# Optimization experiments

Measured on AMD Instinct MI355X. Metric: run time of the kernel, lower is better.

## Reference

```python
import jax, jax.numpy as jnp
from jax import lax
import numpy as np

B, DIM, H, W = 1, 48, 192, 192
HEADS, K, DIL = 2, 7, 3
HD = DIM // HEADS
HID = int(DIM * 2.66)  # 127 (Restormer GEGLU hidden)
EPS = 1e-5


def _window_starts(L, Kk, D):
    # NATTEN window-start rule: keep phase i % D, shift window inside bounds.
    s = np.zeros(L, dtype=np.int32)
    for i in range(L):
        if D <= 1:
            st = max(i - Kk // 2, 0)
            if i + Kk // 2 >= L:
                st = L - Kk
        else:
            st = i - (Kk // 2) * D
            if st < 0:
                st = i % D
            elif i + (Kk // 2) * D >= L:
                imodd = i % D
                a = (L // D) * D
                b = L - a
                if imodd < b:
                    st = L - b + imodd - 2 * (Kk // 2) * D
                else:
                    st = a + imodd - Kk * D
        s[i] = st
    return s


def _nbr_tables(L, Kk, D):
    st = _window_starts(L, Kk, D)
    idx = st[:, None] + np.arange(Kk)[None, :] * D          # [L, K] absolute neighbor idx
    pb = (st - np.arange(L)) // D                            # signed offset of window start (in dilation units)
    pb = pb[:, None] + (Kk - 1) + np.arange(Kk)[None, :]     # [L, K] rpb index in [0, 2K-2]
    return jnp.asarray(idx), jnp.asarray(pb)

IH, PBH = _nbr_tables(H, K, DIL)
IW, PBW = _nbr_tables(W, K, DIL)


def layernorm(x, w, b):  # channel LN on NCHW (WithBias, biased var)
    mu = x.mean(1, keepdims=True)
    var = ((x - mu) ** 2).mean(1, keepdims=True)
    return (x - mu) / jnp.sqrt(var + EPS) * w[None, :, None, None] + b[None, :, None, None]


def na2d(x, qkv_w, qkv_b, rpb, proj_w, proj_b):
    # x: NCHW -> BHWC
    t = x.transpose(0, 2, 3, 1)
    qkv = t @ qkv_w.T + qkv_b                                # [B,H,W,3*DIM]
    qkv = qkv.reshape(B, H, W, 3, HEADS, HD)
    q, k, v = qkv[:, :, :, 0], qkv[:, :, :, 1], qkv[:, :, :, 2]
    q = q * (HD ** -0.5)
    # gather dilated 7x7 neighborhoods: [B, H, K, W, K, heads, hd]
    kn = k[:, IH[:, :, None, None], IW[None, None, :, :]]
    vn = v[:, IH[:, :, None, None], IW[None, None, :, :]]
    attn = jnp.einsum('bijnc,bixjync->bijnxy', q, kn)        # [B,H,W,heads,K,K]
    bias = rpb[:, PBH][:, :, :, PBW]                         # [heads,H,K,W,K]
    attn = attn + bias.transpose(1, 3, 0, 2, 4)
    attn = jax.nn.softmax(attn.reshape(B, H, W, HEADS, K * K), axis=-1)
    attn = attn.reshape(B, H, W, HEADS, K, K)
    out = jnp.einsum('bijnxy,bixjync->bijnc', attn, vn).reshape(B, H, W, DIM)
    out = out @ proj_w.T + proj_b
    return out.transpose(0, 3, 1, 2)


def chan_mod(x, eca_w):  # ECA-style gate: GAP -> 1D conv over channels -> sigmoid
    p = x.mean((2, 3))                                       # [B,C]
    y = lax.conv_general_dilated(p[:, None, :], eca_w[None, None, :], (1,), [(3, 3)],
                                 dimension_numbers=('NCH', 'OIH', 'NCH'))[:, 0, :]
    return jax.nn.sigmoid(y)[:, :, None, None]


def ffn(x, w_in, w_dw, w_out):  # conv-GEGLU
    t = jnp.einsum('bchw,oc->bohw', x, w_in)                 # 1x1: DIM -> 2*HID
    t = lax.conv_general_dilated(t, w_dw, (1, 1), [(1, 1), (1, 1)],
                                 feature_group_count=2 * HID,
                                 dimension_numbers=('NCHW', 'OIHW', 'NCHW'))
    x1, x2 = t[:, :HID], t[:, HID:]
    g = jax.nn.gelu(x1, approximate=False) * x2
    return jnp.einsum('bchw,oc->bohw', g, w_out)             # 1x1: HID -> DIM


def setup_inputs() -> dict:
    key = jax.random.key(0)
    ks = jax.random.split(key, 10)
    d = {
        'x': jax.random.normal(ks[0], (B, DIM, H, W), jnp.float32),
        'ln1_w': jnp.ones((DIM,), jnp.float32),
        'ln1_b': jnp.zeros((DIM,), jnp.float32),
        'qkv_w': jax.random.normal(ks[1], (3 * DIM, DIM), jnp.float32) * 0.05,
        'qkv_b': jnp.zeros((3 * DIM,), jnp.float32),
        'rpb': jax.random.normal(ks[2], (HEADS, 2 * K - 1, 2 * K - 1), jnp.float32) * 0.02,
        'proj_w': jax.random.normal(ks[3], (DIM, DIM), jnp.float32) * 0.05,
        'proj_b': jnp.zeros((DIM,), jnp.float32),
        'eca_w': jax.random.normal(ks[4], (7,), jnp.float32) * 0.1,
        'ln2_w': jnp.ones((DIM,), jnp.float32),
        'ln2_b': jnp.zeros((DIM,), jnp.float32),
        'w_in': jax.random.normal(ks[5], (2 * HID, DIM), jnp.float32) * 0.05,
        'w_dw': jax.random.normal(ks[6], (2 * HID, 1, 3, 3), jnp.float32) * 0.05,
        'w_out': jax.random.normal(ks[7], (DIM, HID), jnp.float32) * 0.05,
    }
    return d


def reference(x, ln1_w, ln1_b, qkv_w, qkv_b, rpb, proj_w, proj_b, eca_w,
              ln2_w, ln2_b, w_in, w_dw, w_out):
    xn1 = layernorm(x, ln1_w, ln1_b)
    x = x + na2d(xn1, qkv_w, qkv_b, rpb, proj_w, proj_b) * chan_mod(xn1, eca_w)
    x = x + ffn(layernorm(x, ln2_w, ln2_b), w_in, w_dw, w_out)
    return x
```

## Files before the change

kernel.cpp:

```cpp
#include <hip/hip_runtime.h>
#include <hip/hip_bf16.h>
#include <math.h>

#define HW_ (192*192)
#define Wd 192
#define HIDc 127
#define NBLK1 (HW_/64)

#define O_LN1W 0
#define O_QKVW 96
#define O_QKVB 7008
#define O_RPB  7152
#define O_PROJW 7490
#define O_PROJB 9794
#define O_ECA  9842
#define O_LN2W 9849
#define O_WIN  9945
#define O_WDW  22137
#define O_WOUT 24423
#define WTS_LEN 30519

typedef unsigned short ushort_t;

__device__ __forceinline__ float b2f(__hip_bfloat16 v){ return __bfloat162float(v); }
__device__ __forceinline__ float u2f(ushort_t h){ return __uint_as_float(((unsigned)h)<<16); }
__device__ __forceinline__ ushort_t f2u(float f){
    __hip_bfloat16 h = __float2bfloat16(f);
    union { __hip_bfloat16 b; ushort_t u; } c; c.b = h; return c.u;
}
__device__ __forceinline__ void up2(unsigned u, float& a, float& b){
    a = __uint_as_float(u << 16);
    b = __uint_as_float(u & 0xffff0000u);
}

__device__ __forceinline__ int wstart(int i){
    if (i < 9) return i % 3;
    if (i >= 183) return 171 + (i % 3);
    return i - 9;
}

__device__ __forceinline__ float dot48bf(const uint4* wr, const float* xr){
    float acc = 0.f;
    #pragma unroll
    for (int c8 = 0; c8 < 6; c8++){
        uint4 u = wr[c8];
        float f0,f1,f2,f3,f4,f5,f6,f7;
        up2(u.x,f0,f1); up2(u.y,f2,f3); up2(u.z,f4,f5); up2(u.w,f6,f7);
        acc += f0*xr[8*c8]   + f1*xr[8*c8+1] + f2*xr[8*c8+2] + f3*xr[8*c8+3]
             + f4*xr[8*c8+4] + f5*xr[8*c8+5] + f6*xr[8*c8+6] + f7*xr[8*c8+7];
    }
    return acc;
}

__global__ void convert_kernel(
    const void* p0, const void* p1, const void* p2, const void* p3,
    const void* p4, const void* p5, const void* p6, const void* p7,
    const void* p8, const void* p9, const void* p10, const void* p11,
    const void* p12, const ushort_t* __restrict__ xu, int* __restrict__ mode_out,
    float* __restrict__ wts, ushort_t* __restrict__ qkvbf, ushort_t* __restrict__ woutTbf,
    ushort_t* __restrict__ winbf, ushort_t* __restrict__ projbf)
{
    __shared__ int sbad;
    if (threadIdx.x == 0) sbad = 0;
    __syncthreads();
    {
        unsigned u = xu[2*threadIdx.x];
        float f = __uint_as_float(u << 16);
        if (!(fabsf(f) < 100.f)) atomicAdd(&sbad, 1);
    }
    __syncthreads();
    const int md = (sbad > 16) ? 1 : 0;
    if (blockIdx.x == 0 && threadIdx.x == 0) mode_out[0] = md;

    const void* ps[13] = {p0,p1,p2,p3,p4,p5,p6,p7,p8,p9,p10,p11,p12};
    const int sz[13]  = {48,48,6912,144,338,2304,48,7,48,48,12192,2286,6096};
    const int off[13] = {O_LN1W,48,O_QKVW,O_QKVB,O_RPB,O_PROJW,O_PROJB,O_ECA,
                         O_LN2W,9897,O_WIN,O_WDW,O_WOUT};
    int b = blockIdx.x;
    if (b >= 13){
        if (b == 13){
            if (md){
                const float* s = (const float*)p2;
                for (int i = threadIdx.x; i < 6912; i += 256) qkvbf[i] = f2u(s[i]);
            } else {
                const ushort_t* s = (const ushort_t*)p2;
                for (int i = threadIdx.x; i < 6912; i += 256) qkvbf[i] = s[i];
            }
        } else if (b == 14){
            if (md){
                const float* s = (const float*)p12;
                for (int i = threadIdx.x; i < 6096; i += 256){
                    int c = i / 48, o = i - c*48;
                    woutTbf[i] = f2u(s[o*127 + c]);
                }
            } else {
                const ushort_t* s = (const ushort_t*)p12;
                for (int i = threadIdx.x; i < 6096; i += 256){
                    int c = i / 48, o = i - c*48;
                    woutTbf[i] = s[o*127 + c];
                }
            }
        } else if (b == 15){
            if (md){
                const float* s = (const float*)p10;
                for (int i = threadIdx.x; i < 12192; i += 256) winbf[i] = f2u(s[i]);
            } else {
                const ushort_t* s = (const ushort_t*)p10;
                for (int i = threadIdx.x; i < 12192; i += 256) winbf[i] = s[i];
            }
        } else {
            if (md){
                const float* s = (const float*)p5;
                for (int i = threadIdx.x; i < 2304; i += 256) projbf[i] = f2u(s[i]);
            } else {
                const ushort_t* s = (const ushort_t*)p5;
                for (int i = threadIdx.x; i < 2304; i += 256) projbf[i] = s[i];
            }
        }
        return;
    }
    int n = sz[b];
    float* dst = wts + off[b];
    if (md){
        const float* s = (const float*)ps[b];
        for (int i = threadIdx.x; i < n; i += 256) dst[i] = s[i];
    } else {
        const __hip_bfloat16* s = (const __hip_bfloat16*)ps[b];
        for (int i = threadIdx.x; i < n; i += 256) dst[i] = b2f(s[i]);
    }
}

__global__ __launch_bounds__(384) void ln1qkv_kernel(
    const void* __restrict__ x, const int* __restrict__ mode,
    const float* __restrict__ wts, const ushort_t* __restrict__ qkvbf,
    ushort_t* __restrict__ q, ushort_t* __restrict__ k, ushort_t* __restrict__ v,
    float* __restrict__ chpart)
{
    __shared__ float sx[64*49];

    const int tid  = threadIdx.x;
    const int px_l = tid & 63;
    const int r6   = __builtin_amdgcn_readfirstlane(tid >> 6);
    const int p0   = blockIdx.x * 64;
    const int p    = p0 + px_l;

    if (mode[0]){
        const float* xf = (const float*)x;
        for (int idx = tid; idx < 64*48; idx += 384){
            int c = idx >> 6, pl = idx & 63;
            sx[pl*49 + c] = xf[c*HW_ + p0 + pl];
        }
    } else {
        const __hip_bfloat16* xb = (const __hip_bfloat16*)x;
        for (int idx = tid; idx < 64*48; idx += 384){
            int c = idx >> 6, pl = idx & 63;
            sx[pl*49 + c] = b2f(xb[c*HW_ + p0 + pl]);
        }
    }
    __syncthreads();

    float xr[48];
    float mu = 0.f;
    #pragma unroll
    for (int c = 0; c < 48; c++){ xr[c] = sx[px_l*49 + c]; mu += xr[c]; }
    mu *= (1.f/48.f);
    float var = 0.f;
    #pragma unroll
    for (int c = 0; c < 48; c++){ float d = xr[c]-mu; var += d*d; }
    var *= (1.f/48.f);
    float rs = rsqrtf(var + 1e-5f);
    #pragma unroll
    for (int c = 0; c < 48; c++)
        xr[c] = (xr[c]-mu)*rs*wts[O_LN1W + c] + wts[O_LN1W + 48 + c];

    if (tid < 64){
        #pragma unroll
        for (int c = 0; c < 48; c++){
            float s = xr[c];
            s += __shfl_xor(s, 1);  s += __shfl_xor(s, 2);  s += __shfl_xor(s, 4);
            s += __shfl_xor(s, 8);  s += __shfl_xor(s, 16); s += __shfl_xor(s, 32);
            if (tid == 0) chpart[blockIdx.x*48 + c] = s;
        }
    }

    const int rbase = r6 * 24;
    const float scale = (r6 < 2) ? 0.20412414523193154f : 1.0f;
    float ov[24];
    #pragma unroll 4
    for (int ro = 0; ro < 24; ro++){
        int r = rbase + ro;
        float acc = wts[O_QKVB + r]
                  + dot48bf((const uint4*)(qkvbf + r*48), xr);
        ov[ro] = acc * scale;
    }

    unsigned int pk[12];
    #pragma unroll
    for (int d = 0; d < 12; d++)
        pk[d] = (unsigned)f2u(ov[2*d]) | ((unsigned)f2u(ov[2*d+1]) << 16);
    ushort_t* tp = (r6 >> 1) == 0 ? q : ((r6 >> 1) == 1 ? k : v);
    uint4* dst4 = (uint4*)(tp + (size_t)p*48 + (r6 & 1)*24);
    dst4[0] = make_uint4(pk[0], pk[1], pk[2],  pk[3]);
    dst4[1] = make_uint4(pk[4], pk[5], pk[6],  pk[7]);
    dst4[2] = make_uint4(pk[8], pk[9], pk[10], pk[11]);
}

__global__ __launch_bounds__(256) void gatered_kernel(
    const float* __restrict__ chpart, float* __restrict__ msum)
{
    __shared__ float red[4];
    const int c = blockIdx.x;
    const int tid = threadIdx.x;
    float acc = 0.f;
    for (int b = tid; b < NBLK1; b += 256)
        acc += chpart[b*48 + c];
    acc += __shfl_xor(acc, 1);  acc += __shfl_xor(acc, 2);  acc += __shfl_xor(acc, 4);
    acc += __shfl_xor(acc, 8);  acc += __shfl_xor(acc, 16); acc += __shfl_xor(acc, 32);
    if ((tid & 63) == 0) red[tid >> 6] = acc;
    __syncthreads();
    if (tid == 0)
        msum[c] = (red[0] + red[1] + red[2] + red[3]) * (1.f / (float)HW_);
}

__global__ void gate_kernel(const float* __restrict__ msum,
                            const float* __restrict__ wts,
                            float* __restrict__ gate)
{
    __shared__ float m[48];
    int t = threadIdx.x;
    if (t < 48) m[t] = msum[t];
    __syncthreads();
    if (t < 48){
        float a = 0.f;
        for (int kk = 0; kk < 7; kk++){
            int cc = t + kk - 3;
            if (cc >= 0 && cc < 48) a += wts[O_ECA + kk] * m[cc];
        }
        gate[t] = 1.f / (1.f + expf(-a));
    }
}

__global__ __launch_bounds__(256) void attn_kernel(
    const ushort_t* __restrict__ q, const ushort_t* __restrict__ k,
    const ushort_t* __restrict__ v, const float* __restrict__ wts,
    ushort_t* __restrict__ aout)
{
    const int head = blockIdx.y;
    __shared__ float srpb[169];
    for (int i = threadIdx.x; i < 169; i += 256) srpb[i] = wts[O_RPB + head*169 + i];
    __syncthreads();

    const int tid    = threadIdx.x;
    const int half   = tid & 1;
    const int parity = (tid >> 1) & 1;
    const int px     = blockIdx.x * 64 + (tid >> 2);
    const int i = px / Wd, j = px % Wd;
    const int sti = wstart(i), stj = wstart(j);
    const int pbi = (sti - i) / 3 + 6;
    const int pbj = (stj - j) / 3 + 6;
    const int choff = head*24 + half*12;

    float qr[12];
    {
        const ushort4* qp = (const ushort4*)(q + (size_t)px*48 + choff);
        #pragma unroll
        for (int b = 0; b < 3; b++){
            ushort4 uu = qp[b];
            qr[4*b]   = u2f(uu.x); qr[4*b+1] = u2f(uu.y);
            qr[4*b+2] = u2f(uu.z); qr[4*b+3] = u2f(uu.w);
        }
    }

    float m = -1e30f, s = 0.f;
    float acc[12];
    #pragma unroll
    for (int c = 0; c < 12; c++) acc[c] = 0.f;

    #pragma unroll
    for (int t = 0; t < 25; t++){
        int n = 2*t + parity;
        const bool inval = (n > 48);
        if (inval) n = 48;
        int xx = (n * 147) >> 10;
        int yy = n - 7*xx;
        int ii = sti + 3*xx, jj = stj + 3*yy;
        const size_t nb = (size_t)(ii*Wd + jj)*48 + choff;
        const ushort4* kp = (const ushort4*)(k + nb);
        const ushort4* vp = (const ushort4*)(v + nb);
        ushort4 k0 = kp[0], k1 = kp[1], k2 = kp[2];
        ushort4 v0 = vp[0], v1 = vp[1], v2 = vp[2];
        float d = qr[0]*u2f(k0.x) + qr[1]*u2f(k0.y)
                + qr[2]*u2f(k0.z) + qr[3]*u2f(k0.w)
                + qr[4]*u2f(k1.x) + qr[5]*u2f(k1.y)
                + qr[6]*u2f(k1.z) + qr[7]*u2f(k1.w)
                + qr[8]*u2f(k2.x) + qr[9]*u2f(k2.y)
                + qr[10]*u2f(k2.z) + qr[11]*u2f(k2.w);
        d += __shfl_xor(d, 1);
        float sc = d + srpb[(pbi+xx)*13 + (pbj+yy)];
        if (inval) sc = -1e30f;
        float mn = fmaxf(m, sc);
        float corr = __expf(m - mn);
        float p = __expf(sc - mn);
        s = s*corr + p;
        m = mn;
        acc[0]  = acc[0] *corr + p*u2f(v0.x);
        acc[1]  = acc[1] *corr + p*u2f(v0.y);
        acc[2]  = acc[2] *corr + p*u2f(v0.z);
        acc[3]  = acc[3] *corr + p*u2f(v0.w);
        acc[4]  = acc[4] *corr + p*u2f(v1.x);
        acc[5]  = acc[5] *corr + p*u2f(v1.y);
        acc[6]  = acc[6] *corr + p*u2f(v1.z);
        acc[7]  = acc[7] *corr + p*u2f(v1.w);
        acc[8]  = acc[8] *corr + p*u2f(v2.x);
        acc[9]  = acc[9] *corr + p*u2f(v2.y);
        acc[10] = acc[10]*corr + p*u2f(v2.z);
        acc[11] = acc[11]*corr + p*u2f(v2.w);
    }

    {
        float mo = __shfl_xor(m, 2);
        float so = __shfl_xor(s, 2);
        float mn = fmaxf(m, mo);
        float ca = __expf(m - mn), cb = __expf(mo - mn);
        s = s*ca + so*cb;
        #pragma unroll
        for (int c = 0; c < 12; c++)
            acc[c] = acc[c]*ca + __shfl_xor(acc[c], 2)*cb;
    }
    const float inv = 1.f / s;
    if (parity == 0){
        #pragma unroll
        for (int c = 0; c < 12; c++)
            aout[(size_t)(choff + c)*HW_ + px] = f2u(acc[c] * inv);
    }
}

__global__ __launch_bounds__(256) void proj_kernel(
    const ushort_t* __restrict__ aout, const float* __restrict__ wts,
    const ushort_t* __restrict__ projbf, const float* __restrict__ gate,
    const void* __restrict__ x, const int* __restrict__ mode,
    float* __restrict__ x2)
{
    const int tid  = threadIdx.x;
    const int px_l = tid & 63;
    const int og   = __builtin_amdgcn_readfirstlane(tid >> 6);
    const int px   = blockIdx.x * 64 + px_l;

    float ar[48];
    #pragma unroll
    for (int c = 0; c < 48; c++) ar[c] = u2f(aout[(size_t)c*HW_ + px]);

    const float* xf = (const float*)x;
    const __hip_bfloat16* xb = (const __hip_bfloat16*)x;
    const int md = mode[0];
    const int ob = og * 12;
    #pragma unroll 2
    for (int oo = 0; oo < 12; oo++){
        int o = ob + oo;
        float acc = wts[O_PROJB + o]
                  + dot48bf((const uint4*)(projbf + o*48), ar);
        float res = md ? xf[o*HW_ + px] : b2f(xb[o*HW_ + px]);
        x2[o*HW_ + px] = res + acc * gate[o];
    }
}

__global__ __launch_bounds__(256) void pw1_kernel(
    const float* __restrict__ x2, const float* __restrict__ wts,
    const ushort_t* __restrict__ winbf, ushort_t* __restrict__ t)
{
    const int tid  = threadIdx.x;
    const int px_l = tid & 63;
    const int og   = __builtin_amdgcn_readfirstlane(tid >> 6);
    const int px   = blockIdx.x * 64 + px_l;

    float xr[48];
    float mu = 0.f;
    #pragma unroll
    for (int c = 0; c < 48; c++){ xr[c] = x2[c*HW_ + px]; mu += xr[c]; }
    mu *= (1.f/48.f);
    float var = 0.f;
    #pragma unroll
    for (int c = 0; c < 48; c++){ float d = xr[c]-mu; var += d*d; }
    var *= (1.f/48.f);
    float rs = rsqrtf(var + 1e-5f);
    #pragma unroll
    for (int c = 0; c < 48; c++)
        xr[c] = (xr[c]-mu)*rs*wts[O_LN2W + c] + wts[O_LN2W + 48 + c];

    const int base = blockIdx.y * 128 + og * 32;
    for (int t2 = 0; t2 < 32; t2 += 2){
        int o0 = base + t2;
        if (o0 >= 254) break;
        const uint4* wA = (const uint4*)(winbf + o0*48);
        const uint4* wB = (const uint4*)(winbf + min(o0+1,253)*48);
        float accA = 0.f, accB = 0.f;
        #pragma unroll
        for (int c8 = 0; c8 < 6; c8++){
            uint4 ua = wA[c8];
            uint4 ub = wB[c8];
            float a0,a1,a2,a3,a4,a5,a6,a7, b0,b1,b2,b3,b4,b5,b6,b7;
            up2(ua.x,a0,a1); up2(ua.y,a2,a3); up2(ua.z,a4,a5); up2(ua.w,a6,a7);
            up2(ub.x,b0,b1); up2(ub.y,b2,b3); up2(ub.z,b4,b5); up2(ub.w,b6,b7);
            accA += a0*xr[8*c8]   + a1*xr[8*c8+1] + a2*xr[8*c8+2] + a3*xr[8*c8+3]
                  + a4*xr[8*c8+4] + a5*xr[8*c8+5] + a6*xr[8*c8+6] + a7*xr[8*c8+7];
            accB += b0*xr[8*c8]   + b1*xr[8*c8+1] + b2*xr[8*c8+2] + b3*xr[8*c8+3]
                  + b4*xr[8*c8+4] + b5*xr[8*c8+5] + b6*xr[8*c8+6] + b7*xr[8*c8+7];
        }
        t[(size_t)o0*HW_ + px] = f2u(accA);
        if (o0+1 < 254) t[(size_t)(o0+1)*HW_ + px] = f2u(accB);
    }
}

__global__ __launch_bounds__(256) void dw_kernel(
    const ushort_t* __restrict__ t, const float* __restrict__ wts,
    ushort_t* __restrict__ g)
{
    const int ch = blockIdx.y;
    const int pp = (blockIdx.x * 256 + threadIdx.x) * 2;
    const int i  = pp / Wd, j = pp % Wd;
    float w1[9], w2[9];
    #pragma unroll
    for (int s = 0; s < 9; s++){
        w1[s] = wts[O_WDW + ch*9 + s];
        w2[s] = wts[O_WDW + (ch+HIDc)*9 + s];
    }
    const ushort_t* t1 = t + (size_t)ch * HW_;
    const ushort_t* t2 = t + (size_t)(ch+HIDc) * HW_;
    float a1x = 0.f, a1y = 0.f, a2x = 0.f, a2y = 0.f;
    #pragma unroll
    for (int di = 0; di < 3; di++){
        int ii = i + di - 1;
        if (ii < 0 || ii >= 192) continue;
        int base = ii*Wd + j;
        float r0 = (j   > 0)   ? u2f(t1[base-1]) : 0.f;
        float r1 = u2f(t1[base]);
        float r2 = u2f(t1[base+1]);
        float r3 = (j+2 < 192) ? u2f(t1[base+2]) : 0.f;
        float s0 = (j   > 0)   ? u2f(t2[base-1]) : 0.f;
        float s1 = u2f(t2[base]);
        float s2 = u2f(t2[base+1]);
        float s3 = (j+2 < 192) ? u2f(t2[base+2]) : 0.f;
        float wa = w1[di*3], wb = w1[di*3+1], wc = w1[di*3+2];
        a1x += wa*r0 + wb*r1 + wc*r2;
        a1y += wa*r1 + wb*r2 + wc*r3;
        wa = w2[di*3]; wb = w2[di*3+1]; wc = w2[di*3+2];
        a2x += wa*s0 + wb*s1 + wc*s2;
        a2y += wa*s1 + wb*s2 + wc*s3;
    }
    float gx = a1x * 0.5f * (1.f + erff(a1x * 0.70710678118654752f)) * a2x;
    float gy = a1y * 0.5f * (1.f + erff(a1y * 0.70710678118654752f)) * a2y;
    unsigned pk = (unsigned)f2u(gx) | ((unsigned)f2u(gy) << 16);
    *(unsigned*)(g + (size_t)ch*HW_ + pp) = pk;
}

__global__ __launch_bounds__(128) void pw2_kernel(
    const ushort_t* __restrict__ g, const ushort_t* __restrict__ woutTbf,
    const float* __restrict__ x2, void* __restrict__ outv,
    const int* __restrict__ mode)
{
    const int ob = blockIdx.y * 12;
    const int p  = blockIdx.x * 128 + threadIdx.x;
    float acc[12];
    #pragma unroll
    for (int o = 0; o < 12; o++) acc[o] = 0.f;
    #pragma unroll 4
    for (int c = 0; c < 127; c++){
        float gv = u2f(g[(size_t)c*HW_ + p]);
        const unsigned* wr = (const unsigned*)(woutTbf + c*48 + ob);
        #pragma unroll
        for (int d = 0; d < 6; d++){
            float w0, w1;
            up2(wr[d], w0, w1);
            acc[2*d]   += w0*gv;
            acc[2*d+1] += w1*gv;
        }
    }
    if (mode[0]){
        float* out = (float*)outv;
        #pragma unroll
        for (int o = 0; o < 12; o++){
            int oc = ob + o;
            out[(size_t)oc*HW_ + p] = x2[(size_t)oc*HW_ + p] + acc[o];
        }
    } else {
        __hip_bfloat16* out = (__hip_bfloat16*)outv;
        #pragma unroll
        for (int o = 0; o < 12; o++){
            int oc = ob + o;
            out[(size_t)oc*HW_ + p] =
                __float2bfloat16(x2[(size_t)oc*HW_ + p] + acc[o]);
        }
    }
}

extern "C" void kernel_launch(void* const* d_in, const int* in_sizes, int n_in,
                              void* d_out, int out_size, void* d_ws, size_t ws_size,
                              hipStream_t stream)
{
    (void)in_sizes; (void)n_in; (void)out_size;

    char* ws = (char*)d_ws;
    ushort_t* q    = (ushort_t*)(ws);
    ushort_t* k    = (ushort_t*)(ws + 3538944);
    ushort_t* v    = (ushort_t*)(ws + 7077888);
    ushort_t* aout = (ushort_t*)(ws + 10616832);
    ushort_t* t    = (ushort_t*)(ws);
    float*    x2   = (float*)   (ws + 18726912);
    ushort_t* g    = (ushort_t*)(ws + 25804800);
    float*    gate = (float*)   (ws + 35168448);
    int*      mode = (int*)     (ws + 35168640);
    float*    wts  = (float*)   (ws + 35168656);
    float*    chpart=(float*)   (ws + 35168656 + (size_t)WTS_LEN*4);
    float*    msum = chpart + (size_t)NBLK1*48;
    ushort_t* qkvbf= (ushort_t*)(msum + 48);
    ushort_t* woutTbf = qkvbf + 6912;
    ushort_t* winbf   = woutTbf + 6096;
    ushort_t* projbf  = winbf + 12192;

    size_t need = 35168656 + (size_t)WTS_LEN*4 + (size_t)NBLK1*48*4 + 48*4
                + (6912 + 6096 + 12192 + 2304)*2;
    if (ws_size < need) return;

    convert_kernel<<<17, 256, 0, stream>>>(
        d_in[1], d_in[2], d_in[3], d_in[4], d_in[5], d_in[6], d_in[7],
        d_in[8], d_in[9], d_in[10], d_in[11], d_in[12], d_in[13],
        (const ushort_t*)d_in[0], mode, wts, qkvbf, woutTbf, winbf, projbf);

    ln1qkv_kernel<<<dim3(NBLK1), 384, 0, stream>>>(d_in[0], mode, wts, qkvbf,
                                                   q, k, v, chpart);
    gatered_kernel<<<48, 256, 0, stream>>>(chpart, msum);
    gate_kernel<<<1, 64, 0, stream>>>(msum, wts, gate);
    attn_kernel<<<dim3(HW_/64, 2), 256, 0, stream>>>(q, k, v, wts, aout);
    proj_kernel<<<dim3(HW_/64), 256, 0, stream>>>(aout, wts, projbf, gate,
                                                  d_in[0], mode, x2);
    pw1_kernel<<<dim3(HW_/64, 2), 256, 0, stream>>>(x2, wts, winbf, t);
    dw_kernel<<<dim3(HW_/512, 127), 256, 0, stream>>>(t, wts, g);
    pw2_kernel<<<dim3(HW_/128, 4), 128, 0, stream>>>(g, woutTbf, x2, d_out, mode);
}
```

Before: 247.6 us.

## Fuse attention with projection, merge gate kernels, widen depthwise conv per thread

Attention and the output projection now run in one kernel. Each thread handles a full head (24 channels) and writes the normalized result to shared memory, which the projection then reads instead of a bf16 global buffer. The channel-mean reduction and the ECA gate are merged into one single-block kernel, which removes one launch but serializes the reduction onto one block. The depthwise conv now computes 4 pixels per thread with vectorized loads. The fused attention kernel roughly doubles register pressure and uses about 13KB of shared memory per block, which may lower occupancy.

```diff
diff --git a/kernel.cpp b/kernel.cpp
--- a/kernel.cpp
+++ b/kernel.cpp
@@ -205,78 +205,76 @@
     dst4[2] = make_uint4(pk[8], pk[9], pk[10], pk[11]);
 }
 
-__global__ __launch_bounds__(256) void gatered_kernel(
-    const float* __restrict__ chpart, float* __restrict__ msum)
-{
-    __shared__ float red[4];
-    const int c = blockIdx.x;
-    const int tid = threadIdx.x;
-    float acc = 0.f;
-    for (int b = tid; b < NBLK1; b += 256)
-        acc += chpart[b*48 + c];
-    acc += __shfl_xor(acc, 1);  acc += __shfl_xor(acc, 2);  acc += __shfl_xor(acc, 4);
-    acc += __shfl_xor(acc, 8);  acc += __shfl_xor(acc, 16); acc += __shfl_xor(acc, 32);
-    if ((tid & 63) == 0) red[tid >> 6] = acc;
-    __syncthreads();
-    if (tid == 0)
-        msum[c] = (red[0] + red[1] + red[2] + red[3]) * (1.f / (float)HW_);
-}
-
-__global__ void gate_kernel(const float* __restrict__ msum,
-                            const float* __restrict__ wts,
-                            float* __restrict__ gate)
-{
-    __shared__ float m[48];
-    int t = threadIdx.x;
-    if (t < 48) m[t] = msum[t];
+__global__ __launch_bounds__(256) void gatefuse_kernel(
+    const float* __restrict__ chpart, const float* __restrict__ wts,
+    float* __restrict__ gate)
+{
+    __shared__ float sm[48];
+    const int t = threadIdx.x;
+    if (t < 192){
+        const int ch = t >> 2, qq = t & 3;
+        float acc = 0.f;
+        #pragma unroll 4
+        for (int b = qq; b < NBLK1; b += 4)
+            acc += chpart[b*48 + ch];
+        acc += __shfl_xor(acc, 1);
+        acc += __shfl_xor(acc, 2);
+        if (qq == 0) sm[ch] = acc * (1.f / (float)HW_);
+    }
     __syncthreads();
     if (t < 48){
         float a = 0.f;
         for (int kk = 0; kk < 7; kk++){
             int cc = t + kk - 3;
-            if (cc >= 0 && cc < 48) a += wts[O_ECA + kk] * m[cc];
+            if (cc >= 0 && cc < 48) a += wts[O_ECA + kk] * sm[cc];
         }
         gate[t] = 1.f / (1.f + expf(-a));
     }
 }
 
-__global__ __launch_bounds__(256) void attn_kernel(
+__global__ __launch_bounds__(256) void attnproj_kernel(
     const ushort_t* __restrict__ q, const ushort_t* __restrict__ k,
     const ushort_t* __restrict__ v, const float* __restrict__ wts,
-    ushort_t* __restrict__ aout)
-{
-    const int head = blockIdx.y;
-    __shared__ float srpb[169];
-    for (int i = threadIdx.x; i < 169; i += 256) srpb[i] = wts[O_RPB + head*169 + i];
+    const ushort_t* __restrict__ projbf, const float* __restrict__ gate,
+    const void* __restrict__ x, const int* __restrict__ mode,
+    float* __restrict__ x2)
+{
+    __shared__ float srpb[338];
+    __shared__ float sa[64*49];
+
+    const int tid = threadIdx.x;
+    for (int i0 = tid; i0 < 338; i0 += 256) srpb[i0] = wts[O_RPB + i0];
     __syncthreads();
 
-    const int tid    = threadIdx.x;
-    const int half   = tid & 1;
-    const int parity = (tid >> 1) & 1;
-    const int px     = blockIdx.x * 64 + (tid >> 2);
+    const int parity = tid & 1;
+    const int head   = (tid >> 1) & 1;
+    const int px_l   = tid >> 2;
+    const int px     = blockIdx.x * 64 + px_l;
     const int i = px / Wd, j = px % Wd;
     const int sti = wstart(i), stj = wstart(j);
     const int pbi = (sti - i) / 3 + 6;
     const int pbj = (stj - j) / 3 + 6;
-    const int choff = head*24 + half*12;
-
-    float qr[12];
+    const int choff = head * 24;
+    const float* rpb = srpb + head*169;
+
+    float qr[24];
     {
-        const ushort4* qp = (const ushort4*)(q + (size_t)px*48 + choff);
-        #pragma unroll
-        for (int b = 0; b < 3; b++){
-            ushort4 uu = qp[b];
-            qr[4*b]   = u2f(uu.x); qr[4*b+1] = u2f(uu.y);
-            qr[4*b+2] = u2f(uu.z); qr[4*b+3] = u2f(uu.w);
-        }
+        const uint4* qp = (const uint4*)(q + (size_t)px*48 + choff);
+        uint4 q0 = qp[0], q1 = qp[1], q2 = qp[2];
+        up2(q0.x,qr[0],qr[1]);   up2(q0.y,qr[2],qr[3]);
+        up2(q0.z,qr[4],qr[5]);   up2(q0.w,qr[6],qr[7]);
+        up2(q1.x,qr[8],qr[9]);   up2(q1.y,qr[10],qr[11]);
+        up2(q1.z,qr[12],qr[13]); up2(q1.w,qr[14],qr[15]);
+        up2(q2.x,qr[16],qr[17]); up2(q2.y,qr[18],qr[19]);
+        up2(q2.z,qr[20],qr[21]); up2(q2.w,qr[22],qr[23]);
     }
 
     float m = -1e30f, s = 0.f;
-    float acc[12];
-    #pragma unroll
-    for (int c = 0; c < 12; c++) acc[c] = 0.f;
-
-    #pragma unroll
+    float acc[24];
+    #pragma unroll
+    for (int c = 0; c < 24; c++) acc[c] = 0.f;
+
+    #pragma unroll 5
     for (int t = 0; t < 25; t++){
         int n = 2*t + parity;
         const bool inval = (n > 48);
@@ -285,70 +283,75 @@
         int yy = n - 7*xx;
         int ii = sti + 3*xx, jj = stj + 3*yy;
         const size_t nb = (size_t)(ii*Wd + jj)*48 + choff;
-        const ushort4* kp = (const ushort4*)(k + nb);
-        const ushort4* vp = (const ushort4*)(v + nb);
-        ushort4 k0 = kp[0], k1 = kp[1], k2 = kp[2];
-        ushort4 v0 = vp[0], v1 = vp[1], v2 = vp[2];
-        float d = qr[0]*u2f(k0.x) + qr[1]*u2f(k0.y)
-                + qr[2]*u2f(k0.z) + qr[3]*u2f(k0.w)
-                + qr[4]*u2f(k1.x) + qr[5]*u2f(k1.y)
-                + qr[6]*u2f(k1.z) + qr[7]*u2f(k1.w)
-                + qr[8]*u2f(k2.x) + qr[9]*u2f(k2.y)
-                + qr[10]*u2f(k2.z) + qr[11]*u2f(k2.w);
-        d += __shfl_xor(d, 1);
-        float sc = d + srpb[(pbi+xx)*13 + (pbj+yy)];
+        const uint4* kp = (const uint4*)(k + nb);
+        const uint4* vp = (const uint4*)(v + nb);
+        uint4 K0 = kp[0], K1 = kp[1], K2 = kp[2];
+        uint4 V0 = vp[0], V1 = vp[1], V2 = vp[2];
+        float a, b;
+        float d = 0.f;
+        up2(K0.x,a,b); d += qr[0]*a  + qr[1]*b;
+        up2(K0.y,a,b); d += qr[2]*a  + qr[3]*b;
+        up2(K0.z,a,b); d += qr[4]*a  + qr[5]*b;
+        up2(K0.w,a,b); d += qr[6]*a  + qr[7]*b;
+        up2(K1.x,a,b); d += qr[8]*a  + qr[9]*b;
+        up2(K1.y,a,b); d += qr[10]*a + qr[11]*b;
+        up2(K1.z,a,b); d += qr[12]*a + qr[13]*b;
+        up2(K1.w,a,b); d += qr[14]*a + qr[15]*b;
+        up2(K2.x,a,b); d += qr[16]*a + qr[17]*b;
+        up2(K2.y,a,b); d += qr[18]*a + qr[19]*b;
+        up2(K2.z,a,b); d += qr[20]*a + qr[21]*b;
+        up2(K2.w,a,b); d += qr[22]*a + qr[23]*b;
+        float sc = d + rpb[(pbi+xx)*13 + (pbj+yy)];
         if (inval) sc = -1e30f;
         float mn = fmaxf(m, sc);
         float corr = __expf(m - mn);
         float p = __expf(sc - mn);
         s = s*corr + p;
         m = mn;
-        acc[0]  = acc[0] *corr + p*u2f(v0.x);
-        acc[1]  = acc[1] *corr + p*u2f(v0.y);
-        acc[2]  = acc[2] *corr + p*u2f(v0.z);
-        acc[3]  = acc[3] *corr + p*u2f(v0.w);
-        acc[4]  = acc[4] *corr + p*u2f(v1.x);
-        acc[5]  = acc[5] *corr + p*u2f(v1.y);
-        acc[6]  = acc[6] *corr + p*u2f(v1.z);
-        acc[7]  = acc[7] *corr + p*u2f(v1.w);
-        acc[8]  = acc[8] *corr + p*u2f(v2.x);
-        acc[9]  = acc[9] *corr + p*u2f(v2.y);
-        acc[10] = acc[10]*corr + p*u2f(v2.z);
-        acc[11] = acc[11]*corr + p*u2f(v2.w);
+        up2(V0.x,a,b); acc[0] =acc[0] *corr + p*a; acc[1] =acc[1] *corr + p*b;
+        up2(V0.y,a,b); acc[2] =acc[2] *corr + p*a; acc[3] =acc[3] *corr + p*b;
+        up2(V0.z,a,b); acc[4] =acc[4] *corr + p*a; acc[5] =acc[5] *corr + p*b;
+        up2(V0.w,a,b); acc[6] =acc[6] *corr + p*a; acc[7] =acc[7] *corr + p*b;
+        up2(V1.x,a,b); acc[8] =acc[8] *corr + p*a; acc[9] =acc[9] *corr + p*b;
+        up2(V1.y,a,b); acc[10]=acc[10]*corr + p*a; acc[11]=acc[11]*corr + p*b;
+        up2(V1.z,a,b); acc[12]=acc[12]*corr + p*a; acc[13]=acc[13]*corr + p*b;
+        up2(V1.w,a,b); acc[14]=acc[14]*corr + p*a; acc[15]=acc[15]*corr + p*b;
+        up2(V2.x,a,b); acc[16]=acc[16]*corr + p*a; acc[17]=acc[17]*corr + p*b;
+        up2(V2.y,a,b); acc[18]=acc[18]*corr + p*a; acc[19]=acc[19]*corr + p*b;
+        up2(V2.z,a,b); acc[20]=acc[20]*corr + p*a; acc[21]=acc[21]*corr + p*b;
+        up2(V2.w,a,b); acc[22]=acc[22]*corr + p*a; acc[23]=acc[23]*corr + p*b;
     }
 
     {
-        float mo = __shfl_xor(m, 2);
-        float so = __shfl_xor(s, 2);
+        float mo = __shfl_xor(m, 1);
+        float so = __shfl_xor(s, 1);
         float mn = fmaxf(m, mo);
         float ca = __expf(m - mn), cb = __expf(mo - mn);
         s = s*ca + so*cb;
         #pragma unroll
-        for (int c = 0; c < 12; c++)
-            acc[c] = acc[c]*ca + __shfl_xor(acc[c], 2)*cb;
+        for (int c = 0; c < 24; c++)
+            acc[c] = acc[c]*ca + __shfl_xor(acc[c], 1)*cb;
     }
     const float inv = 1.f / s;
-    if (parity == 0){
-        #pragma unroll
-        for (int c = 0; c < 12; c++)
-            aout[(size_t)(choff + c)*HW_ + px] = f2u(acc[c] * inv);
-    }
-}
-
-__global__ __launch_bounds__(256) void proj_kernel(
-    const ushort_t* __restrict__ aout, const float* __restrict__ wts,
-    const ushort_t* __restrict__ projbf, const float* __restrict__ gate,
-    const void* __restrict__ x, const int* __restrict__ mode,
-    float* __restrict__ x2)
-{
-    const int tid  = threadIdx.x;
-    const int px_l = tid & 63;
-    const int og   = __builtin_amdgcn_readfirstlane(tid >> 6);
-    const int px   = blockIdx.x * 64 + px_l;
+    {
+        float* dst = sa + px_l*49 + choff + parity*12;
+        if (parity == 0){
+            #pragma unroll
+            for (int c = 0; c < 12; c++) dst[c] = acc[c] * inv;
+        } else {
+            #pragma unroll
+            for (int c = 0; c < 12; c++) dst[c] = acc[12 + c] * inv;
+        }
+    }
+    __syncthreads();
+
+    const int px_l2 = tid & 63;
+    const int og    = __builtin_amdgcn_readfirstlane(tid >> 6);
+    const int px2   = blockIdx.x * 64 + px_l2;
 
     float ar[48];
     #pragma unroll
-    for (int c = 0; c < 48; c++) ar[c] = u2f(aout[(size_t)c*HW_ + px]);
+    for (int c = 0; c < 48; c++) ar[c] = sa[px_l2*49 + c];
 
     const float* xf = (const float*)x;
     const __hip_bfloat16* xb = (const __hip_bfloat16*)x;
@@ -357,10 +360,10 @@
     #pragma unroll 2
     for (int oo = 0; oo < 12; oo++){
         int o = ob + oo;
-        float acc = wts[O_PROJB + o]
-                  + dot48bf((const uint4*)(projbf + o*48), ar);
-        float res = md ? xf[o*HW_ + px] : b2f(xb[o*HW_ + px]);
-        x2[o*HW_ + px] = res + acc * gate[o];
+        float accp = wts[O_PROJB + o]
+                   + dot48bf((const uint4*)(projbf + o*48), ar);
+        float res = md ? xf[o*HW_ + px2] : b2f(xb[o*HW_ + px2]);
+        x2[o*HW_ + px2] = res + accp * gate[o];
     }
 }
 
@@ -416,41 +419,55 @@
     ushort_t* __restrict__ g)
 {
     const int ch = blockIdx.y;
-    const int pp = (blockIdx.x * 256 + threadIdx.x) * 2;
+    const int pp = (blockIdx.x * 256 + threadIdx.x) * 4;
     const int i  = pp / Wd, j = pp % Wd;
     float w1[9], w2[9];
     #pragma unroll
-    for (int s = 0; s < 9; s++){
-        w1[s] = wts[O_WDW + ch*9 + s];
-        w2[s] = wts[O_WDW + (ch+HIDc)*9 + s];
+    for (int s2 = 0; s2 < 9; s2++){
+        w1[s2] = wts[O_WDW + ch*9 + s2];
+        w2[s2] = wts[O_WDW + (ch+HIDc)*9 + s2];
     }
     const ushort_t* t1 = t + (size_t)ch * HW_;
     const ushort_t* t2 = t + (size_t)(ch+HIDc) * HW_;
-    float a1x = 0.f, a1y = 0.f, a2x = 0.f, a2y = 0.f;
+    float a10=0.f,a11=0.f,a12=0.f,a13=0.f;
+    float a20=0.f,a21=0.f,a22=0.f,a23=0.f;
     #pragma unroll
     for (int di = 0; di < 3; di++){
         int ii = i + di - 1;
         if (ii < 0 || ii >= 192) continue;
         int base = ii*Wd + j;
-        float r0 = (j   > 0)   ? u2f(t1[base-1]) : 0.f;
-        float r1 = u2f(t1[base]);
-        float r2 = u2f(t1[base+1]);
-        float r3 = (j+2 < 192) ? u2f(t1[base+2]) : 0.f;
-        float s0 = (j   > 0)   ? u2f(t2[base-1]) : 0.f;
-        float s1 = u2f(t2[base]);
-        float s2 = u2f(t2[base+1]);
-        float s3 = (j+2 < 192) ? u2f(t2[base+2]) : 0.f;
         float wa = w1[di*3], wb = w1[di*3+1], wc = w1[di*3+2];
-        a1x += wa*r0 + wb*r1 + wc*r2;
-        a1y += wa*r1 + wb*r2 + wc*r3;
+        {
+            uint2 mm = *(const uint2*)(t1 + base);
+            float c0,c1,c2,c3; up2(mm.x,c0,c1); up2(mm.y,c2,c3);
+            float cm = (j > 0)     ? u2f(t1[base-1]) : 0.f;
+            float cp = (j+4 < Wd)  ? u2f(t1[base+4]) : 0.f;
+            a10 += wa*cm + wb*c0 + wc*c1;
+            a11 += wa*c0 + wb*c1 + wc*c2;
+            a12 += wa*c1 + wb*c2 + wc*c3;
+            a13 += wa*c2 + wb*c3 + wc*cp;
+        }
         wa = w2[di*3]; wb = w2[di*3+1]; wc = w2[di*3+2];
-        a2x += wa*s0 + wb*s1 + wc*s2;
-        a2y += wa*s1 + wb*s2 + wc*s3;
-    }
-    float gx = a1x * 0.5f * (1.f + erff(a1x * 0.70710678118654752f)) * a2x;
-    float gy = a1y * 0.5f * (1.f + erff(a1y * 0.70710678118654752f)) * a2y;
-    unsigned pk = (unsigned)f2u(gx) | ((unsigned)f2u(gy) << 16);
-    *(unsigned*)(g + (size_t)ch*HW_ + pp) = pk;
+        {
+            uint2 mm = *(const uint2*)(t2 + base);
+            float c0,c1,c2,c3; up2(mm.x,c0,c1); up2(mm.y,c2,c3);
+            float cm = (j > 0)     ? u2f(t2[base-1]) : 0.f;
+            float cp = (j+4 < Wd)  ? u2f(t2[base+4]) : 0.f;
+            a20 += wa*cm + wb*c0 + wc*c1;
+            a21 += wa*c0 + wb*c1 + wc*c2;
+            a22 += wa*c1 + wb*c2 + wc*c3;
+            a23 += wa*c2 + wb*c3 + wc*cp;
+        }
+    }
+    const float RS2 = 0.70710678118654752f;
+    float g0 = a10 * 0.5f * (1.f + erff(a10 * RS2)) * a20;
+    float g1 = a11 * 0.5f * (1.f + erff(a11 * RS2)) * a21;
+    float g2 = a12 * 0.5f * (1.f + erff(a12 * RS2)) * a22;
+    float g3 = a13 * 0.5f * (1.f + erff(a13 * RS2)) * a23;
+    uint2 pk;
+    pk.x = (unsigned)f2u(g0) | ((unsigned)f2u(g1) << 16);
+    pk.y = (unsigned)f2u(g2) | ((unsigned)f2u(g3) << 16);
+    *(uint2*)(g + (size_t)ch*HW_ + pp) = pk;
 }
 
 __global__ __launch_bounds__(128) void pw2_kernel(
@@ -503,7 +520,6 @@
     ushort_t* q    = (ushort_t*)(ws);
     ushort_t* k    = (ushort_t*)(ws + 3538944);
     ushort_t* v    = (ushort_t*)(ws + 7077888);
-    ushort_t* aout = (ushort_t*)(ws + 10616832);
     ushort_t* t    = (ushort_t*)(ws);
     float*    x2   = (float*)   (ws + 18726912);
     ushort_t* g    = (ushort_t*)(ws + 25804800);
@@ -528,12 +544,10 @@
 
     ln1qkv_kernel<<<dim3(NBLK1), 384, 0, stream>>>(d_in[0], mode, wts, qkvbf,
                                                    q, k, v, chpart);
-    gatered_kernel<<<48, 256, 0, stream>>>(chpart, msum);
-    gate_kernel<<<1, 64, 0, stream>>>(msum, wts, gate);
-    attn_kernel<<<dim3(HW_/64, 2), 256, 0, stream>>>(q, k, v, wts, aout);
-    proj_kernel<<<dim3(HW_/64), 256, 0, stream>>>(aout, wts, projbf, gate,
-                                                  d_in[0], mode, x2);
+    gatefuse_kernel<<<1, 256, 0, stream>>>(chpart, wts, gate);
+    attnproj_kernel<<<dim3(HW_/64), 256, 0, stream>>>(q, k, v, wts, projbf, gate,
+                                                      d_in[0], mode, x2);
     pw1_kernel<<<dim3(HW_/64, 2), 256, 0, stream>>>(x2, wts, winbf, t);
-    dw_kernel<<<dim3(HW_/512, 127), 256, 0, stream>>>(t, wts, g);
+    dw_kernel<<<dim3(HW_/1024, 127), 256, 0, stream>>>(t, wts, g);
     pw2_kernel<<<dim3(HW_/128, 4), 128, 0, stream>>>(g, woutTbf, x2, d_out, mode);
 }
```

Result: faster. 239.6 us (-3.2%).
